# Performance work log

Hardware: AMD Instinct MI355X
Metric: run time of the kernel (lower is better)

The kernel has to match this reference:

```python
import jax, jax.numpy as jnp
import numpy as np

SIGMA = 1.0
EPS = 1e-08


def setup_inputs() -> dict:
    key = jax.random.key(0)
    k1, k2 = jax.random.split(key)
    N, D = 8192, 768
    sentence_representation = jax.random.normal(k1, (N, D), dtype=jnp.float32)
    labels = jax.random.randint(k2, (N,), 0, 2, dtype=jnp.int64)
    return {"sentence_representation": sentence_representation, "labels": labels}


def reference(sentence_representation, labels):
    x = sentence_representation
    norm = jnp.sum(x * x, axis=1, keepdims=True)  # [N,1]
    # squared euclidean distances [N,N]
    distances = norm + norm.T - 2.0 * jnp.matmul(x, x.T)
    fuzzy_relation = jnp.exp(-distances / (2.0 * SIGMA ** 2))
    # one_hot @ one_hot.T == 1 where labels match (hard labels)
    label_similarity = (labels[:, None] == labels[None, :]).astype(fuzzy_relation.dtype)
    positive_sum = jnp.sum(fuzzy_relation * label_similarity, axis=1)
    all_sum = jnp.sum(fuzzy_relation, axis=1)
    loss = -jnp.log(positive_sum / (all_sum + EPS))
    return jnp.mean(loss)
```

## Files before the change

### kernel.cpp

```cpp
#include <hip/hip_runtime.h>
#include <hip/hip_bf16.h>


#define NROWS 8192
#define DIM   768
#define BM    128
#define BKB   128
#define NKS   (DIM / BKB)
#define NBLK  (NROWS / BM)
#define NTILES (NBLK * (NBLK + 1) / 2)
#define QS    20.0f
#define SCL2  (1.4426950408889634f / (2.0f * QS * QS))

typedef __attribute__((ext_vector_type(4))) int   int4v;
typedef __attribute__((ext_vector_type(4))) float f32x4;

__device__ __forceinline__ void gload_lds16(const void* g, void* l) {
  __builtin_amdgcn_global_load_lds(
      (const __attribute__((address_space(1))) void*)g,
      (__attribute__((address_space(3))) void*)l, 16, 0, 0);
}

__global__ void prep_kernel(const float* __restrict__ x,
                            unsigned char* __restrict__ xq,
                            int* __restrict__ normsI,
                            float* __restrict__ part) {
  if (blockIdx.x < 16)
    ((float4*)part)[blockIdx.x * 256 + threadIdx.x] = make_float4(0.f, 0.f, 0.f, 0.f);
  const int row  = blockIdx.x * 4 + (threadIdx.x >> 6);
  const int lane = threadIdx.x & 63;
  const float* xr = x + (size_t)row * DIM + lane * 12;
  int nacc = 0;
  unsigned w[3];
  #pragma unroll
  for (int c = 0; c < 3; ++c) {
    float4 v = *(const float4*)(xr + c * 4);
    int q0 = __float2int_rn(fminf(fmaxf(v.x * QS, -127.f), 127.f));
    int q1 = __float2int_rn(fminf(fmaxf(v.y * QS, -127.f), 127.f));
    int q2 = __float2int_rn(fminf(fmaxf(v.z * QS, -127.f), 127.f));
    int q3 = __float2int_rn(fminf(fmaxf(v.w * QS, -127.f), 127.f));
    nacc += q0 * q0 + q1 * q1 + q2 * q2 + q3 * q3;
    w[c] = (q0 & 255) | ((q1 & 255) << 8) | ((q2 & 255) << 16) | ((q3 & 255) << 24);
  }
  unsigned* out = (unsigned*)(xq + (size_t)row * DIM) + lane * 3;
  out[0] = w[0]; out[1] = w[1]; out[2] = w[2];
  #pragma unroll
  for (int off = 32; off; off >>= 1) nacc += __shfl_down(nacc, off);
  if (lane == 0) normsI[row] = nacc;
}

__global__ __launch_bounds__(256, 3)
void fused_kernel(const unsigned char* __restrict__ xq,
                  const int* __restrict__ normsI,
                  const int* __restrict__ labels,
                  float* __restrict__ part) {
  const int orig = blockIdx.x;
  const int t = (orig & 7) * (NTILES / 8) + (orig >> 3);
  int bi = (int)(((double)(2 * NBLK + 1) -
                  sqrt((double)(2 * NBLK + 1) * (2 * NBLK + 1) - 8.0 * t)) * 0.5);
  while ((bi + 1) * (2 * NBLK - bi) / 2 <= t) ++bi;
  while (bi * (2 * NBLK - bi + 1) / 2 > t) --bi;
  const int bj = bi + (t - bi * (2 * NBLK - bi + 1) / 2);
  const bool diag = (bi == bj);

  __shared__ unsigned char sA[BM * BKB];
  __shared__ unsigned char sB[BM * BKB];

  const int tid  = threadIdx.x;
  const int lane = tid & 63;
  const int wid  = tid >> 6;
  const int wm   = wid >> 1, wn = wid & 1;
  const int ln15 = lane & 15, hi4 = lane >> 4;
  const int s7   = ln15 & 7;
  const int brow = bi * BM;
  const int bcol = bj * BM;

  int srcoff[4], dstoff[4];
  #pragma unroll
  for (int i = 0; i < 4; ++i) {
    int c = i * 256 + tid;
    int r = c >> 3, u = c & 7;
    srcoff[i] = r * DIM + ((u ^ (r & 7)) << 4);
    dstoff[i] = c << 4;
  }
  const unsigned char* gA = xq + (size_t)brow * DIM;
  const unsigned char* gB = xq + (size_t)bcol * DIM;

  int4v zero = {0, 0, 0, 0};
  int4v acc[4][4];
  #pragma unroll
  for (int mi = 0; mi < 4; ++mi)
    #pragma unroll
    for (int nj = 0; nj < 4; ++nj) acc[mi][nj] = zero;

  for (int ks = 0; ks < NKS; ++ks) {
    const int kb = ks * BKB;
    #pragma unroll
    for (int i = 0; i < 4; ++i) {
      gload_lds16(gA + srcoff[i] + kb, sA + dstoff[i]);
      gload_lds16(gB + srcoff[i] + kb, sB + dstoff[i]);
    }
    __syncthreads();
    #pragma unroll
    for (int kk = 0; kk < 2; ++kk) {
      const int slot = (((kk << 2) | hi4) ^ s7) << 4;
      int4v af[4], bf[4];
      #pragma unroll
      for (int mi = 0; mi < 4; ++mi)
        af[mi] = *(const int4v*)&sA[(wm * 64 + mi * 16 + ln15) * BKB + slot];
      #pragma unroll
      for (int nj = 0; nj < 4; ++nj)
        bf[nj] = *(const int4v*)&sB[(wn * 64 + nj * 16 + ln15) * BKB + slot];
      #pragma unroll
      for (int mi = 0; mi < 4; ++mi)
        #pragma unroll
        for (int nj = 0; nj < 4; ++nj)
          acc[mi][nj] = __builtin_amdgcn_mfma_i32_16x16x64_i8(
              af[mi], bf[nj], acc[mi][nj], 0, 0, 0);
    }
    __syncthreads();
  }

  int njn[4], lc[4];
  float fc1[4], fc0[4];
  #pragma unroll
  for (int nj = 0; nj < 4; ++nj) {
    int col = bcol + wn * 64 + nj * 16 + ln15;
    njn[nj] = normsI[col];
    lc[nj] = labels[col];
    fc1[nj] = (float)lc[nj]; fc0[nj] = 1.0f - fc1[nj];
  }
  float cs0[4] = {0.f, 0.f, 0.f, 0.f}, cs1[4] = {0.f, 0.f, 0.f, 0.f};

  float* redr = (float*)sA;
  float* redc = (float*)sB;

  #pragma unroll
  for (int mi = 0; mi < 4; ++mi) {
    const int rbase = brow + wm * 64 + mi * 16 + hi4 * 4;
    const int4 niv = *(const int4*)&normsI[rbase];
    const int4 lv  = *(const int4*)&labels[rbase];
    float lr1[4] = { (float)lv.x, (float)lv.y, (float)lv.z, (float)lv.w };
    const int nimin = min(min(niv.x, niv.y), min(niv.z, niv.w));
    float rs0[4] = {0.f, 0.f, 0.f, 0.f}, rs1[4] = {0.f, 0.f, 0.f, 0.f};
    #pragma unroll
    for (int nj = 0; nj < 4; ++nj) {
      int4v a = acc[mi][nj];
      int vmax = max(max(a[0], a[1]), max(a[2], a[3]));
      int d2max = (vmax << 1) - nimin - njn[nj];
      if ((float)d2max * SCL2 > -30.f) {
        int nin[4] = { niv.x, niv.y, niv.z, niv.w };
        #pragma unroll
        for (int r = 0; r < 4; ++r) {
          int d2 = (a[r] << 1) - nin[r] - njn[nj];
          float f = __builtin_amdgcn_exp2f((float)d2 * SCL2);
          rs1[r] = fmaf(f, fc1[nj], rs1[r]);
          rs0[r] = fmaf(f, fc0[nj], rs0[r]);
          cs1[nj] = fmaf(f, lr1[r], cs1[nj]);
          cs0[nj] = fmaf(f, 1.0f - lr1[r], cs0[nj]);
        }
      }
    }
    #pragma unroll
    for (int r = 0; r < 4; ++r) {
      float a = rs0[r], b = rs1[r];
      #pragma unroll
      for (int off = 1; off < 16; off <<= 1) {
        a += __shfl_xor(a, off);
        b += __shfl_xor(b, off);
      }
      if (ln15 == 0) {
        int row_l = wm * 64 + mi * 16 + hi4 * 4 + r;
        float pos = (lr1[r] != 0.f) ? b : a;
        redr[(wn * 128 + row_l) * 2 + 0] = pos;
        redr[(wn * 128 + row_l) * 2 + 1] = a + b;
      }
    }
  }

  if (!diag) {
    #pragma unroll
    for (int nj = 0; nj < 4; ++nj) {
      float a = cs0[nj], b = cs1[nj];
      a += __shfl_xor(a, 16); a += __shfl_xor(a, 32);
      b += __shfl_xor(b, 16); b += __shfl_xor(b, 32);
      if (hi4 == 0) {
        int col_l = wn * 64 + nj * 16 + ln15;
        float pos = lc[nj] ? b : a;
        redc[(wm * 128 + col_l) * 2 + 0] = pos;
        redc[(wm * 128 + col_l) * 2 + 1] = a + b;
      }
    }
  }
  __syncthreads();
  if (tid < BM) {
    atomicAdd(&part[2 * (brow + tid) + 0], redr[tid * 2 + 0] + redr[(128 + tid) * 2 + 0]);
    atomicAdd(&part[2 * (brow + tid) + 1], redr[tid * 2 + 1] + redr[(128 + tid) * 2 + 1]);
    if (!diag) {
      atomicAdd(&part[2 * (bcol + tid) + 0], redc[tid * 2 + 0] + redc[(128 + tid) * 2 + 0]);
      atomicAdd(&part[2 * (bcol + tid) + 1], redc[tid * 2 + 1] + redc[(128 + tid) * 2 + 1]);
    }
  }
}

__global__ void loss_kernel(const float* __restrict__ part,
                            float* __restrict__ out) {
  int tid = threadIdx.x;
  float sum = 0.f;
  for (int row = tid; row < NROWS; row += 1024) {
    float pos = part[2 * row], all = part[2 * row + 1];
    sum += -logf(pos / (all + 1e-8f));
  }
  for (int off = 32; off; off >>= 1) sum += __shfl_down(sum, off);
  __shared__ float w[16];
  if ((tid & 63) == 0) w[tid >> 6] = sum;
  __syncthreads();
  if (tid == 0) {
    float t = 0.f;
    for (int i = 0; i < 16; ++i) t += w[i];
    out[0] = t / (float)NROWS;
  }
}

extern "C" void kernel_launch(void* const* d_in, const int* in_sizes, int n_in,
                              void* d_out, int out_size, void* d_ws, size_t ws_size,
                              hipStream_t stream) {
  const float* x      = (const float*)d_in[0];
  const int*   labels = (const int*)d_in[1];
  char* ws = (char*)d_ws;

  const size_t xq_bytes    = (size_t)NROWS * DIM;
  const size_t norms_bytes = (size_t)NROWS * 4;
  const size_t part_bytes  = (size_t)NROWS * 2 * 4;
  if (ws_size < xq_bytes + norms_bytes + part_bytes) return;

  unsigned char* xq = (unsigned char*)ws;
  int*   normsI = (int*)(ws + xq_bytes);
  float* part   = (float*)(ws + xq_bytes + norms_bytes);

  prep_kernel<<<NROWS / 4, 256, 0, stream>>>(x, xq, normsI, part);
  fused_kernel<<<NTILES, 256, 0, stream>>>(xq, normsI, labels, part);
  loss_kernel<<<1, 1024, 0, stream>>>(part, (float*)d_out);
}
```

Before: 63.93 us.

## Load MFMA operands directly from global memory, dropping LDS staging and barriers

The int8 GEMM main loop no longer stages A/B tiles through shared memory with global_load_lds and two barriers per k-step. Each wave now reads its MFMA fragments straight from global memory (16-byte loads per lane), and the k-loop is unrolled by two to allow overlap. Shared memory is cut down to the small reduction buffers, which could raise occupancy. In exchange, each fragment is loaded redundantly by the two waves that share it, global traffic rises, and the per-lane loads are strided by DIM and so less coalesced, leaning on L1/L2 hit rates.

```diff
diff --git a/kernel.cpp b/kernel.cpp
--- a/kernel.cpp
+++ b/kernel.cpp
@@ -5,8 +5,7 @@
 #define NROWS 8192
 #define DIM   768
 #define BM    128
-#define BKB   128
-#define NKS   (DIM / BKB)
+#define NKS   6
 #define NBLK  (NROWS / BM)
 #define NTILES (NBLK * (NBLK + 1) / 2)
 #define QS    20.0f
@@ -14,12 +13,6 @@
 
 typedef __attribute__((ext_vector_type(4))) int   int4v;
 typedef __attribute__((ext_vector_type(4))) float f32x4;
-
-__device__ __forceinline__ void gload_lds16(const void* g, void* l) {
-  __builtin_amdgcn_global_load_lds(
-      (const __attribute__((address_space(1))) void*)g,
-      (__attribute__((address_space(3))) void*)l, 16, 0, 0);
-}
 
 __global__ void prep_kernel(const float* __restrict__ x,
                             unsigned char* __restrict__ xq,
@@ -63,28 +56,19 @@
   const int bj = bi + (t - bi * (2 * NBLK - bi + 1) / 2);
   const bool diag = (bi == bj);
 
-  __shared__ unsigned char sA[BM * BKB];
-  __shared__ unsigned char sB[BM * BKB];
+  __shared__ float redr[2][BM][2];
+  __shared__ float redc[2][BM][2];
 
   const int tid  = threadIdx.x;
   const int lane = tid & 63;
   const int wid  = tid >> 6;
   const int wm   = wid >> 1, wn = wid & 1;
   const int ln15 = lane & 15, hi4 = lane >> 4;
-  const int s7   = ln15 & 7;
   const int brow = bi * BM;
   const int bcol = bj * BM;
 
-  int srcoff[4], dstoff[4];
-  #pragma unroll
-  for (int i = 0; i < 4; ++i) {
-    int c = i * 256 + tid;
-    int r = c >> 3, u = c & 7;
-    srcoff[i] = r * DIM + ((u ^ (r & 7)) << 4);
-    dstoff[i] = c << 4;
-  }
-  const unsigned char* gA = xq + (size_t)brow * DIM;
-  const unsigned char* gB = xq + (size_t)bcol * DIM;
+  const unsigned char* pA = xq + (size_t)(brow + wm * 64 + ln15) * DIM + hi4 * 16;
+  const unsigned char* pB = xq + (size_t)(bcol + wn * 64 + ln15) * DIM + hi4 * 16;
 
   int4v zero = {0, 0, 0, 0};
   int4v acc[4][4];
@@ -93,32 +77,28 @@
     #pragma unroll
     for (int nj = 0; nj < 4; ++nj) acc[mi][nj] = zero;
 
+  #pragma unroll 2
   for (int ks = 0; ks < NKS; ++ks) {
-    const int kb = ks * BKB;
-    #pragma unroll
-    for (int i = 0; i < 4; ++i) {
-      gload_lds16(gA + srcoff[i] + kb, sA + dstoff[i]);
-      gload_lds16(gB + srcoff[i] + kb, sB + dstoff[i]);
-    }
-    __syncthreads();
-    #pragma unroll
-    for (int kk = 0; kk < 2; ++kk) {
-      const int slot = (((kk << 2) | hi4) ^ s7) << 4;
-      int4v af[4], bf[4];
-      #pragma unroll
-      for (int mi = 0; mi < 4; ++mi)
-        af[mi] = *(const int4v*)&sA[(wm * 64 + mi * 16 + ln15) * BKB + slot];
-      #pragma unroll
-      for (int nj = 0; nj < 4; ++nj)
-        bf[nj] = *(const int4v*)&sB[(wn * 64 + nj * 16 + ln15) * BKB + slot];
+    const int kb = ks * 128;
+    int4v af[4][2], bf[4][2];
+    #pragma unroll
+    for (int mi = 0; mi < 4; ++mi) {
+      af[mi][0] = *(const int4v*)(pA + mi * 16 * DIM + kb);
+      af[mi][1] = *(const int4v*)(pA + mi * 16 * DIM + kb + 64);
+    }
+    #pragma unroll
+    for (int nj = 0; nj < 4; ++nj) {
+      bf[nj][0] = *(const int4v*)(pB + nj * 16 * DIM + kb);
+      bf[nj][1] = *(const int4v*)(pB + nj * 16 * DIM + kb + 64);
+    }
+    #pragma unroll
+    for (int kk = 0; kk < 2; ++kk)
       #pragma unroll
       for (int mi = 0; mi < 4; ++mi)
         #pragma unroll
         for (int nj = 0; nj < 4; ++nj)
           acc[mi][nj] = __builtin_amdgcn_mfma_i32_16x16x64_i8(
-              af[mi], bf[nj], acc[mi][nj], 0, 0, 0);
-    }
-    __syncthreads();
+              af[mi][kk], bf[nj][kk], acc[mi][nj], 0, 0, 0);
   }
 
   int njn[4], lc[4];
@@ -131,9 +111,6 @@
     fc1[nj] = (float)lc[nj]; fc0[nj] = 1.0f - fc1[nj];
   }
   float cs0[4] = {0.f, 0.f, 0.f, 0.f}, cs1[4] = {0.f, 0.f, 0.f, 0.f};
-
-  float* redr = (float*)sA;
-  float* redc = (float*)sB;
 
   #pragma unroll
   for (int mi = 0; mi < 4; ++mi) {
@@ -172,8 +149,8 @@
       if (ln15 == 0) {
         int row_l = wm * 64 + mi * 16 + hi4 * 4 + r;
         float pos = (lr1[r] != 0.f) ? b : a;
-        redr[(wn * 128 + row_l) * 2 + 0] = pos;
-        redr[(wn * 128 + row_l) * 2 + 1] = a + b;
+        redr[wn][row_l][0] = pos;
+        redr[wn][row_l][1] = a + b;
       }
     }
   }
@@ -187,18 +164,18 @@
       if (hi4 == 0) {
         int col_l = wn * 64 + nj * 16 + ln15;
         float pos = lc[nj] ? b : a;
-        redc[(wm * 128 + col_l) * 2 + 0] = pos;
-        redc[(wm * 128 + col_l) * 2 + 1] = a + b;
+        redc[wm][col_l][0] = pos;
+        redc[wm][col_l][1] = a + b;
       }
     }
   }
   __syncthreads();
   if (tid < BM) {
-    atomicAdd(&part[2 * (brow + tid) + 0], redr[tid * 2 + 0] + redr[(128 + tid) * 2 + 0]);
-    atomicAdd(&part[2 * (brow + tid) + 1], redr[tid * 2 + 1] + redr[(128 + tid) * 2 + 1]);
+    atomicAdd(&part[2 * (brow + tid) + 0], redr[0][tid][0] + redr[1][tid][0]);
+    atomicAdd(&part[2 * (brow + tid) + 1], redr[0][tid][1] + redr[1][tid][1]);
     if (!diag) {
-      atomicAdd(&part[2 * (bcol + tid) + 0], redc[tid * 2 + 0] + redc[(128 + tid) * 2 + 0]);
-      atomicAdd(&part[2 * (bcol + tid) + 1], redc[tid * 2 + 1] + redc[(128 + tid) * 2 + 1]);
+      atomicAdd(&part[2 * (bcol + tid) + 0], redc[0][tid][0] + redc[1][tid][0]);
+      atomicAdd(&part[2 * (bcol + tid) + 1], redc[0][tid][1] + redc[1][tid][1]);
     }
   }
 }
```

New measurement: 126.9 us. 1.98x slower.

## Use 256-row tiles with 1024-thread blocks and double-buffered LDS loads

Applied to the files above, without the earlier changes.

Doubles the output tile to 256x256, runs 16 waves per block in a 4x4 layout, and double-buffers the int8 K-slices in LDS so the next slice loads while MFMAs run on the current one. The aim is less global and LDS traffic per MFMA and load latency hidden behind compute. The cost is 128KB of LDS per block, so only one block fits per CU. Only 528 tiles remain, leaving a poor tail across the CUs. The launch bound of (1024,4) may also force a very tight register budget and cause spills.

```diff
diff --git a/kernel.cpp b/kernel.cpp
--- a/kernel.cpp
+++ b/kernel.cpp
@@ -4,7 +4,7 @@
 
 #define NROWS 8192
 #define DIM   768
-#define BM    128
+#define BM    256
 #define BKB   128
 #define NKS   (DIM / BKB)
 #define NBLK  (NROWS / BM)
@@ -49,7 +49,7 @@
   if (lane == 0) normsI[row] = nacc;
 }
 
-__global__ __launch_bounds__(256, 3)
+__global__ __launch_bounds__(1024, 4)
 void fused_kernel(const unsigned char* __restrict__ xq,
                   const int* __restrict__ normsI,
                   const int* __restrict__ labels,
@@ -63,22 +63,22 @@
   const int bj = bi + (t - bi * (2 * NBLK - bi + 1) / 2);
   const bool diag = (bi == bj);
 
-  __shared__ unsigned char sA[BM * BKB];
-  __shared__ unsigned char sB[BM * BKB];
+  __shared__ unsigned char sh[2][2][BM * BKB];
 
   const int tid  = threadIdx.x;
   const int lane = tid & 63;
   const int wid  = tid >> 6;
-  const int wm   = wid >> 1, wn = wid & 1;
+  const int wr   = wid >> 2;
+  const int wc   = wid & 3;
   const int ln15 = lane & 15, hi4 = lane >> 4;
   const int s7   = ln15 & 7;
   const int brow = bi * BM;
   const int bcol = bj * BM;
 
-  int srcoff[4], dstoff[4];
-  #pragma unroll
-  for (int i = 0; i < 4; ++i) {
-    int c = i * 256 + tid;
+  int srcoff[2], dstoff[2];
+  #pragma unroll
+  for (int i = 0; i < 2; ++i) {
+    int c = i * 1024 + tid;
     int r = c >> 3, u = c & 7;
     srcoff[i] = r * DIM + ((u ^ (r & 7)) << 4);
     dstoff[i] = c << 4;
@@ -93,51 +93,61 @@
     #pragma unroll
     for (int nj = 0; nj < 4; ++nj) acc[mi][nj] = zero;
 
+  #pragma unroll
+  for (int i = 0; i < 2; ++i) {
+    gload_lds16(gA + srcoff[i], &sh[0][0][dstoff[i]]);
+    gload_lds16(gB + srcoff[i], &sh[0][1][dstoff[i]]);
+  }
+  __syncthreads();
+
   for (int ks = 0; ks < NKS; ++ks) {
-    const int kb = ks * BKB;
-    #pragma unroll
-    for (int i = 0; i < 4; ++i) {
-      gload_lds16(gA + srcoff[i] + kb, sA + dstoff[i]);
-      gload_lds16(gB + srcoff[i] + kb, sB + dstoff[i]);
-    }
-    __syncthreads();
+    const int p = ks & 1;
+    if (ks + 1 < NKS) {
+      const int kb = (ks + 1) * BKB;
+      #pragma unroll
+      for (int i = 0; i < 2; ++i) {
+        gload_lds16(gA + srcoff[i] + kb, &sh[p ^ 1][0][dstoff[i]]);
+        gload_lds16(gB + srcoff[i] + kb, &sh[p ^ 1][1][dstoff[i]]);
+      }
+    }
+    const unsigned char* bufA = sh[p][0];
+    const unsigned char* bufB = sh[p][1];
     #pragma unroll
     for (int kk = 0; kk < 2; ++kk) {
       const int slot = (((kk << 2) | hi4) ^ s7) << 4;
-      int4v af[4], bf[4];
-      #pragma unroll
-      for (int mi = 0; mi < 4; ++mi)
-        af[mi] = *(const int4v*)&sA[(wm * 64 + mi * 16 + ln15) * BKB + slot];
+      int4v bf[4];
       #pragma unroll
       for (int nj = 0; nj < 4; ++nj)
-        bf[nj] = *(const int4v*)&sB[(wn * 64 + nj * 16 + ln15) * BKB + slot];
-      #pragma unroll
-      for (int mi = 0; mi < 4; ++mi)
+        bf[nj] = *(const int4v*)&bufB[(wc * 64 + nj * 16 + ln15) * BKB + slot];
+      #pragma unroll
+      for (int mi = 0; mi < 4; ++mi) {
+        int4v af = *(const int4v*)&bufA[(wr * 64 + mi * 16 + ln15) * BKB + slot];
         #pragma unroll
         for (int nj = 0; nj < 4; ++nj)
           acc[mi][nj] = __builtin_amdgcn_mfma_i32_16x16x64_i8(
-              af[mi], bf[nj], acc[mi][nj], 0, 0, 0);
+              af, bf[nj], acc[mi][nj], 0, 0, 0);
+      }
     }
     __syncthreads();
   }
+
+  float* redr = (float*)&sh[0][0][0];
+  float* redc = redr + 4 * 256 * 2;
 
   int njn[4], lc[4];
   float fc1[4], fc0[4];
   #pragma unroll
   for (int nj = 0; nj < 4; ++nj) {
-    int col = bcol + wn * 64 + nj * 16 + ln15;
+    int col = bcol + wc * 64 + nj * 16 + ln15;
     njn[nj] = normsI[col];
     lc[nj] = labels[col];
     fc1[nj] = (float)lc[nj]; fc0[nj] = 1.0f - fc1[nj];
   }
   float cs0[4] = {0.f, 0.f, 0.f, 0.f}, cs1[4] = {0.f, 0.f, 0.f, 0.f};
 
-  float* redr = (float*)sA;
-  float* redc = (float*)sB;
-
   #pragma unroll
   for (int mi = 0; mi < 4; ++mi) {
-    const int rbase = brow + wm * 64 + mi * 16 + hi4 * 4;
+    const int rbase = brow + wr * 64 + mi * 16 + hi4 * 4;
     const int4 niv = *(const int4*)&normsI[rbase];
     const int4 lv  = *(const int4*)&labels[rbase];
     float lr1[4] = { (float)lv.x, (float)lv.y, (float)lv.z, (float)lv.w };
@@ -170,36 +180,47 @@
         b += __shfl_xor(b, off);
       }
       if (ln15 == 0) {
-        int row_l = wm * 64 + mi * 16 + hi4 * 4 + r;
+        int row_l = wr * 64 + mi * 16 + hi4 * 4 + r;
         float pos = (lr1[r] != 0.f) ? b : a;
-        redr[(wn * 128 + row_l) * 2 + 0] = pos;
-        redr[(wn * 128 + row_l) * 2 + 1] = a + b;
-      }
-    }
-  }
-
-  if (!diag) {
-    #pragma unroll
-    for (int nj = 0; nj < 4; ++nj) {
-      float a = cs0[nj], b = cs1[nj];
-      a += __shfl_xor(a, 16); a += __shfl_xor(a, 32);
-      b += __shfl_xor(b, 16); b += __shfl_xor(b, 32);
-      if (hi4 == 0) {
-        int col_l = wn * 64 + nj * 16 + ln15;
-        float pos = lc[nj] ? b : a;
-        redc[(wm * 128 + col_l) * 2 + 0] = pos;
-        redc[(wm * 128 + col_l) * 2 + 1] = a + b;
-      }
+        redr[(wc * 256 + row_l) * 2 + 0] = pos;
+        redr[(wc * 256 + row_l) * 2 + 1] = a + b;
+      }
+    }
+  }
+
+  #pragma unroll
+  for (int nj = 0; nj < 4; ++nj) {
+    float a = cs0[nj], b = cs1[nj];
+    a += __shfl_xor(a, 16); a += __shfl_xor(a, 32);
+    b += __shfl_xor(b, 16); b += __shfl_xor(b, 32);
+    if (hi4 == 0) {
+      int col_l = wc * 64 + nj * 16 + ln15;
+      float pos = lc[nj] ? b : a;
+      redc[(wr * 256 + col_l) * 2 + 0] = pos;
+      redc[(wr * 256 + col_l) * 2 + 1] = a + b;
     }
   }
   __syncthreads();
-  if (tid < BM) {
-    atomicAdd(&part[2 * (brow + tid) + 0], redr[tid * 2 + 0] + redr[(128 + tid) * 2 + 0]);
-    atomicAdd(&part[2 * (brow + tid) + 1], redr[tid * 2 + 1] + redr[(128 + tid) * 2 + 1]);
-    if (!diag) {
-      atomicAdd(&part[2 * (bcol + tid) + 0], redc[tid * 2 + 0] + redc[(128 + tid) * 2 + 0]);
-      atomicAdd(&part[2 * (bcol + tid) + 1], redc[tid * 2 + 1] + redc[(128 + tid) * 2 + 1]);
-    }
+
+  if (tid < 256) {
+    float pos = 0.f, all = 0.f;
+    #pragma unroll
+    for (int g = 0; g < 4; ++g) {
+      pos += redr[(g * 256 + tid) * 2 + 0];
+      all += redr[(g * 256 + tid) * 2 + 1];
+    }
+    atomicAdd(&part[2 * (brow + tid) + 0], pos);
+    atomicAdd(&part[2 * (brow + tid) + 1], all);
+  } else if (tid < 512 && !diag) {
+    const int c = tid - 256;
+    float pos = 0.f, all = 0.f;
+    #pragma unroll
+    for (int g = 0; g < 4; ++g) {
+      pos += redc[(g * 256 + c) * 2 + 0];
+      all += redc[(g * 256 + c) * 2 + 1];
+    }
+    atomicAdd(&part[2 * (bcol + c) + 0], pos);
+    atomicAdd(&part[2 * (bcol + c) + 1], all);
   }
 }
 
@@ -239,6 +260,6 @@
   float* part   = (float*)(ws + xq_bytes + norms_bytes);
 
   prep_kernel<<<NROWS / 4, 256, 0, stream>>>(x, xq, normsI, part);
-  fused_kernel<<<NTILES, 256, 0, stream>>>(xq, normsI, labels, part);
+  fused_kernel<<<NTILES, 1024, 0, stream>>>(xq, normsI, labels, part);
   loss_kernel<<<1, 1024, 0, stream>>>(part, (float*)d_out);
 }
```

Result: slower. 79.01 us (+23.6%).
